# Optimization experiments

Measured on AMD Instinct MI355X. Metric: run time of the kernel, lower is better.

The kernel has to match this reference:

```python
import jax, jax.numpy as jnp
import numpy as np

B = 8388608  # batch

def moth(x, a, b):
    # per-feature parametric elementwise activation: a * x * sigmoid(b * x)
    return a * x * jax.nn.sigmoid(b * x)

def setup_inputs() -> dict:
    key = jax.random.key(0)
    ks = jax.random.split(key, 12)
    inp = {
        'x':  jax.random.normal(ks[0], (B, 2), dtype=jnp.float32),
        'W1': jax.random.normal(ks[1], (2, 8), dtype=jnp.float32) * (1.0 / np.sqrt(2)),
        'b1': jax.random.normal(ks[2], (8,), dtype=jnp.float32) * 0.01,
        'a1': jax.random.normal(ks[3], (8,), dtype=jnp.float32) * 0.1 + 1.0,
        'c1': jax.random.normal(ks[4], (8,), dtype=jnp.float32) * 0.1 + 1.0,
        'W2': jax.random.normal(ks[5], (8, 4), dtype=jnp.float32) * (1.0 / np.sqrt(8)),
        'b2': jax.random.normal(ks[6], (4,), dtype=jnp.float32) * 0.01,
        'a2': jax.random.normal(ks[7], (4,), dtype=jnp.float32) * 0.1 + 1.0,
        'c2': jax.random.normal(ks[8], (4,), dtype=jnp.float32) * 0.1 + 1.0,
        'W3': jax.random.normal(ks[9], (4, 1), dtype=jnp.float32) * (1.0 / np.sqrt(4)),
        'b3': jax.random.normal(ks[10], (1,), dtype=jnp.float32) * 0.01,
    }
    return inp

def reference(x, W1, b1, a1, c1, W2, b2, a2, c2, W3, b3):
    h = x @ W1 + b1            # [B, 8]
    h = moth(h, a1, c1)        # [B, 8]
    h = h @ W2 + b2            # [B, 4]
    h = moth(h, a2, c2)        # [B, 4]
    out = h @ W3 + b3          # [B, 1]
    return out
```

## Files before the change

### kernel.cpp

```cpp
#include <hip/hip_runtime.h>

#define NLOG2E -1.44269504088896340736f

typedef float f32x2 __attribute__((ext_vector_type(2)));


__global__ void prefold_kernel(
    const float* __restrict__ W1, const float* __restrict__ b1,
    const float* __restrict__ a1, const float* __restrict__ c1,
    const float* __restrict__ W2, const float* __restrict__ b2,
    const float* __restrict__ a2, const float* __restrict__ c2,
    const float* __restrict__ W3, const float* __restrict__ b3,
    float* __restrict__ C)
{
    if (threadIdx.x == 0 && blockIdx.x == 0) {
        for (int j = 0; j < 8; ++j) {
            float ncl = c1[j] * NLOG2E;
            C[j]      = W1[j]     * ncl;
            C[8 + j]  = W1[8 + j] * ncl;
            C[16 + j] = b1[j]     * ncl;
            float k1 = a1[j] / ncl;
            for (int k = 0; k < 4; ++k)
                C[24 + j * 4 + k] = W2[j * 4 + k] * k1;
        }
        for (int k = 0; k < 4; ++k) {
            C[56 + k] = b2[k];
            C[60 + k] = c2[k] * NLOG2E;
            C[64 + k] = a2[k] * W3[k];
        }
        C[68] = b3[0];
    }
}

__global__ __launch_bounds__(256, 4) void PlaygroundModel_66365834658304_kernel(
    const float* __restrict__ x, const float* __restrict__ C,
    float* __restrict__ out, int rows)
{
    const f32x2* Cp  = (const f32x2*)C;
    float bb3 = C[68];

    int tid = blockIdx.x * blockDim.x + threadIdx.x;
    long long base = (long long)tid * 4;

    if (base + 3 < rows) {
        const float4* x4 = (const float4*)x;
        float4 p0 = x4[(size_t)tid * 2 + 0];
        float4 p1 = x4[(size_t)tid * 2 + 1];
        float X0[4] = {p0.x, p0.z, p1.x, p1.z};
        float X1[4] = {p0.y, p0.w, p1.y, p1.w};

        f32x2 u[4][4];
#pragma unroll
        for (int r = 0; r < 4; ++r) {
            f32x2 x0b = {X0[r], X0[r]};
            f32x2 x1b = {X1[r], X1[r]};
#pragma unroll
            for (int p = 0; p < 4; ++p)
                u[r][p] = __builtin_elementwise_fma(
                              x0b, Cp[p],
                              __builtin_elementwise_fma(x1b, Cp[4 + p],
                                                        Cp[8 + p]));
        }

#pragma unroll
        for (int r = 0; r < 4; ++r)
#pragma unroll
            for (int p = 0; p < 4; ++p) {
                f32x2 e;
                e[0] = __builtin_amdgcn_exp2f(u[r][p][0]);
                e[1] = __builtin_amdgcn_exp2f(u[r][p][1]);
                f32x2 d = e + 1.0f;
                f32x2 s;
                s[0] = __builtin_amdgcn_rcpf(d[0]);
                s[1] = __builtin_amdgcn_rcpf(d[1]);
                u[r][p] *= s;
            }

        f32x2 t2a[4], t2b[4];
#pragma unroll
        for (int r = 0; r < 4; ++r) {
            f32x2 ta = Cp[28], tb = Cp[29];
#pragma unroll
            for (int j = 0; j < 8; ++j) {
                float hj = u[r][j >> 1][j & 1];
                f32x2 hb = {hj, hj};
                ta = __builtin_elementwise_fma(hb, Cp[12 + j * 2 + 0], ta);
                tb = __builtin_elementwise_fma(hb, Cp[12 + j * 2 + 1], tb);
            }
            t2a[r] = ta; t2b[r] = tb;
        }

        float res[4];
#pragma unroll
        for (int r = 0; r < 4; ++r) {
            f32x2 u2a = Cp[30] * t2a[r];
            f32x2 u2b = Cp[31] * t2b[r];
            f32x2 ea, eb;
            ea[0] = __builtin_amdgcn_exp2f(u2a[0]);
            ea[1] = __builtin_amdgcn_exp2f(u2a[1]);
            eb[0] = __builtin_amdgcn_exp2f(u2b[0]);
            eb[1] = __builtin_amdgcn_exp2f(u2b[1]);
            f32x2 da = ea + 1.0f, db = eb + 1.0f;
            f32x2 sa, sb;
            sa[0] = __builtin_amdgcn_rcpf(da[0]);
            sa[1] = __builtin_amdgcn_rcpf(da[1]);
            sb[0] = __builtin_amdgcn_rcpf(db[0]);
            sb[1] = __builtin_amdgcn_rcpf(db[1]);
            f32x2 pa = t2a[r] * sa;
            f32x2 pb = t2b[r] * sb;
            f32x2 acc = {bb3, 0.0f};
            acc = __builtin_elementwise_fma(pa, Cp[32], acc);
            acc = __builtin_elementwise_fma(pb, Cp[33], acc);
            res[r] = acc[0] + acc[1];
        }
        ((float4*)out)[tid] = make_float4(res[0], res[1], res[2], res[3]);
    } else if (base < rows) {
        const float* uw0  = C;
        const float* uw1  = C + 8;
        const float* ub   = C + 16;
        const float* w2f  = C + 24;
        const float* bb2  = C + 56;
        const float* ncl2 = C + 60;
        const float* aw2  = C + 64;
        for (long long rr = base; rr < rows; ++rr) {
            float x0 = x[rr * 2 + 0], x1 = x[rr * 2 + 1];
            float h[8];
#pragma unroll
            for (int j = 0; j < 8; ++j) {
                float uu = fmaf(x0, uw0[j], fmaf(x1, uw1[j], ub[j]));
                float s  = __builtin_amdgcn_rcpf(
                               1.0f + __builtin_amdgcn_exp2f(uu));
                h[j] = uu * s;
            }
            float o = bb3;
#pragma unroll
            for (int k = 0; k < 4; ++k) {
                float t = bb2[k];
#pragma unroll
                for (int j = 0; j < 8; ++j) t = fmaf(h[j], w2f[j * 4 + k], t);
                float u2 = ncl2[k] * t;
                float sg = __builtin_amdgcn_rcpf(
                               1.0f + __builtin_amdgcn_exp2f(u2));
                o = fmaf(t * sg, aw2[k], o);
            }
            out[rr] = o;
        }
    }
}

extern "C" void kernel_launch(void* const* d_in, const int* in_sizes, int n_in,
                              void* d_out, int out_size, void* d_ws, size_t ws_size,
                              hipStream_t stream) {
    const float* x  = (const float*)d_in[0];
    const float* W1 = (const float*)d_in[1];
    const float* b1 = (const float*)d_in[2];
    const float* a1 = (const float*)d_in[3];
    const float* c1 = (const float*)d_in[4];
    const float* W2 = (const float*)d_in[5];
    const float* b2 = (const float*)d_in[6];
    const float* a2 = (const float*)d_in[7];
    const float* c2 = (const float*)d_in[8];
    const float* W3 = (const float*)d_in[9];
    const float* b3 = (const float*)d_in[10];
    float* out = (float*)d_out;
    float* C   = (float*)d_ws;

    prefold_kernel<<<1, 64, 0, stream>>>(W1, b1, a1, c1, W2, b2, a2, c2,
                                         W3, b3, C);

    int rows  = in_sizes[0] / 2;
    int rows4 = (rows + 3) / 4;
    int block = 256;
    int grid  = (rows4 + block - 1) / block;

    PlaygroundModel_66365834658304_kernel<<<grid, block, 0, stream>>>(
        x, C, out, rows);
}
```

Measured before the change: 126.5 us.

## Fuse constant prefold into main kernel via per-block shared memory

```diff
diff --git a/kernel.cpp b/kernel.cpp
--- a/kernel.cpp
+++ b/kernel.cpp
@@ -5,39 +5,41 @@
 typedef float f32x2 __attribute__((ext_vector_type(2)));
 
 
-__global__ void prefold_kernel(
+__global__ __launch_bounds__(256, 3) void PlaygroundModel_66365834658304_kernel(
+    const float* __restrict__ x,
     const float* __restrict__ W1, const float* __restrict__ b1,
     const float* __restrict__ a1, const float* __restrict__ c1,
     const float* __restrict__ W2, const float* __restrict__ b2,
     const float* __restrict__ a2, const float* __restrict__ c2,
     const float* __restrict__ W3, const float* __restrict__ b3,
-    float* __restrict__ C)
+    float* __restrict__ out, int rows)
 {
-    if (threadIdx.x == 0 && blockIdx.x == 0) {
+    __shared__ __align__(16) float Cs[70];
+
+    if (threadIdx.x == 0) {
+#pragma unroll
         for (int j = 0; j < 8; ++j) {
             float ncl = c1[j] * NLOG2E;
-            C[j]      = W1[j]     * ncl;
-            C[8 + j]  = W1[8 + j] * ncl;
-            C[16 + j] = b1[j]     * ncl;
+            Cs[j]      = W1[j]     * ncl;
+            Cs[8 + j]  = W1[8 + j] * ncl;
+            Cs[16 + j] = b1[j]     * ncl;
             float k1 = a1[j] / ncl;
+#pragma unroll
             for (int k = 0; k < 4; ++k)
-                C[24 + j * 4 + k] = W2[j * 4 + k] * k1;
+                Cs[24 + j * 4 + k] = W2[j * 4 + k] * k1;
         }
+#pragma unroll
         for (int k = 0; k < 4; ++k) {
-            C[56 + k] = b2[k];
-            C[60 + k] = c2[k] * NLOG2E;
-            C[64 + k] = a2[k] * W3[k];
+            Cs[56 + k] = b2[k];
+            Cs[60 + k] = c2[k] * NLOG2E;
+            Cs[64 + k] = a2[k] * W3[k];
         }
-        C[68] = b3[0];
+        Cs[68] = b3[0];
     }
-}
+    __syncthreads();
 
-__global__ __launch_bounds__(256, 4) void PlaygroundModel_66365834658304_kernel(
-    const float* __restrict__ x, const float* __restrict__ C,
-    float* __restrict__ out, int rows)
-{
-    const f32x2* Cp  = (const f32x2*)C;
-    float bb3 = C[68];
+    const f32x2* Cp = (const f32x2*)Cs;
+    float bb3 = Cs[68];
 
     int tid = blockIdx.x * blockDim.x + threadIdx.x;
     long long base = (long long)tid * 4;
@@ -115,13 +117,13 @@
         }
         ((float4*)out)[tid] = make_float4(res[0], res[1], res[2], res[3]);
     } else if (base < rows) {
-        const float* uw0  = C;
-        const float* uw1  = C + 8;
-        const float* ub   = C + 16;
-        const float* w2f  = C + 24;
-        const float* bb2  = C + 56;
-        const float* ncl2 = C + 60;
-        const float* aw2  = C + 64;
+        const float* uw0  = Cs;
+        const float* uw1  = Cs + 8;
+        const float* ub   = Cs + 16;
+        const float* w2f  = Cs + 24;
+        const float* bb2  = Cs + 56;
+        const float* ncl2 = Cs + 60;
+        const float* aw2  = Cs + 64;
         for (long long rr = base; rr < rows; ++rr) {
             float x0 = x[rr * 2 + 0], x1 = x[rr * 2 + 1];
             float h[8];
@@ -163,10 +165,7 @@
     const float* W3 = (const float*)d_in[9];
     const float* b3 = (const float*)d_in[10];
     float* out = (float*)d_out;
-    float* C   = (float*)d_ws;
-
-    prefold_kernel<<<1, 64, 0, stream>>>(W1, b1, a1, c1, W2, b2, a2, c2,
-                                         W3, b3, C);
+    (void)d_ws; (void)ws_size;
 
     int rows  = in_sizes[0] / 2;
     int rows4 = (rows + 3) / 4;
@@ -174,5 +173,5 @@
     int grid  = (rows4 + block - 1) / block;
 
     PlaygroundModel_66365834658304_kernel<<<grid, block, 0, stream>>>(
-        x, C, out, rows);
+        x, W1, b1, a1, c1, W2, b2, a2, c2, W3, b3, out, rows);
 }
```

Result: slower. 131.4 us (+3.9%).
